# Kernel tuning notes

Hardware: AMD Instinct MI355X
Metric: run time of the kernel (lower is better)

## Reference

```python
import jax, jax.numpy as jnp
import numpy as np

B, S, D, H = 4, 1024, 1024, 16
DH = D // H
LN_EPS = 1e-5


def setup_inputs() -> dict:
    key = jax.random.key(0)
    ks = jax.random.split(key, 12)
    lim = 1.0 / np.sqrt(D)
    u = lambda k, shp: jax.random.uniform(k, shp, jnp.float32, -lim, lim)
    return {
        "x": jax.random.normal(ks[0], (B, S, D), jnp.float32),
        "Wq": u(ks[1], (D, D)), "bq": u(ks[2], (D,)),
        "Wk": u(ks[3], (D, D)), "bk": u(ks[4], (D,)),
        "Wv": u(ks[5], (D, D)), "bv": u(ks[6], (D,)),
        "Wo": u(ks[7], (D, D)), "bo": u(ks[8], (D,)),
        "gamma": jnp.ones((D,), jnp.float32),
        "beta": jnp.zeros((D,), jnp.float32),
    }


def _layer_norm(x, gamma, beta):
    mu = jnp.mean(x, axis=-1, keepdims=True)
    var = jnp.mean(jnp.square(x - mu), axis=-1, keepdims=True)
    return (x - mu) * jax.lax.rsqrt(var + LN_EPS) * gamma + beta


def reference(x, Wq, bq, Wk, bk, Wv, bv, Wo, bo, gamma, beta):
    # Linear projections (torch Linear: x @ W^T + b)
    Q = x @ Wq.T + bq  # [B, S, D]
    K = x @ Wk.T + bk
    V = x @ Wv.T + bv
    # Faithful to original: raw view(B*H, S, DH) with NO head transpose
    Q = Q.reshape(B * H, S, DH)
    K = K.reshape(B * H, S, DH)
    V = V.reshape(B * H, S, DH)
    scale = DH ** -0.5
    attn = jnp.einsum('bqd,bkd->bqk', Q, K) * scale  # [B*H, S, S]
    attn = jax.nn.softmax(attn, axis=-1)
    ctx = jnp.einsum('bqk,bkd->bqd', attn, V)  # [B*H, S, DH]
    ctx = ctx.reshape(B, S, D)
    out = ctx @ Wo.T + bo
    out = out + x  # residual (dropout p=0.0 is identity)
    return _layer_norm(out, gamma, beta)
```

## Files before the change

### kernel.cpp

```cpp
#include <hip/hip_runtime.h>
#include <hip/hip_bf16.h>


using u16 = unsigned short;
typedef __attribute__((ext_vector_type(8))) short bf16x8;
typedef __attribute__((ext_vector_type(4))) float f32x4;
typedef __attribute__((ext_vector_type(4))) u16  u16x4;
typedef __attribute__((ext_vector_type(8))) u16  u16x8;

#define AS1C(p) ((const __attribute__((address_space(1))) void*)(p))
#define AS3(p)  ((__attribute__((address_space(3))) void*)(p))

__device__ __forceinline__ u16 f2bf(float f) {
  union { float f; unsigned u; } v; v.f = f;
  unsigned u = v.u;
  return (u16)((u + 0x7fffu + ((u >> 16) & 1u)) >> 16);
}

__device__ __forceinline__ f32x4 mfma16(bf16x8 a, bf16x8 b, f32x4 c) {
  return __builtin_amdgcn_mfma_f32_16x16x32_bf16(a, b, c, 0, 0, 0);
}

__global__ __launch_bounds__(256) void prep_kernel(
    const float* __restrict__ x,
    const float* __restrict__ wq, const float* __restrict__ wk,
    const float* __restrict__ wv, const float* __restrict__ wo,
    const float* __restrict__ bq, const float* __restrict__ bk, const float* __restrict__ bv,
    u16* __restrict__ xb, u16* __restrict__ wb, float* __restrict__ bc)
{
  int ch = blockIdx.x * 256 + threadIdx.x;
  if (ch < 2097152) {
    const float* src; u16* dst;
    if (ch < 1048576) { src = x + ch * 4; dst = xb + ch * 4; }
    else {
      int c2 = ch - 1048576;
      int wsel = c2 >> 18;
      int off  = c2 & 262143;
      const float* wsrc[4] = { wq, wk, wv, wo };
      src = wsrc[wsel] + off * 4;
      dst = wb + wsel * 1048576 + off * 4;
    }
    f32x4 v = *(const f32x4*)src;
    u16x4 o;
    o[0] = f2bf(v[0]); o[1] = f2bf(v[1]); o[2] = f2bf(v[2]); o[3] = f2bf(v[3]);
    *(u16x4*)dst = o;
  } else {
    int c3 = ch - 2097152;
    int bsel = c3 >> 8, off = c3 & 255;
    const float* bsrc[3] = { bq, bk, bv };
    f32x4 v = *(const f32x4*)(bsrc[bsel] + off * 4);
    *(f32x4*)(bc + bsel * 1024 + off * 4) = v;
  }
}

template <int MODE>
__global__ __launch_bounds__(256) void gemm_p4(
    const u16* __restrict__ A, const u16* __restrict__ Bw,
    const float* __restrict__ bias, const float* __restrict__ resid,
    u16* __restrict__ outb, float* __restrict__ outf)
{
  __shared__ u16 As[3][4096];
  __shared__ u16 Bs[3][4096];

  const int K = 1024;
  int tid = threadIdx.x, w = tid >> 6, lane = tid & 63;
  int g = lane >> 4, lr = lane & 15;
  int wr = w >> 1, wcn = w & 1;

  int bid = blockIdx.x;
  int bm = (bid & 7) + 8 * ((bid >> 3) & 3);
  int bn = bid >> 5;

  int ch0 = tid, ch1 = tid + 256;
  auto srcoff = [&](int ch) -> size_t {
    int r = ch >> 2, pc = ch & 3;
    int gc = pc ^ ((r >> 2) & 3);
    return (size_t)r * K + gc * 8;
  };
  const u16* aS0 = A  + (size_t)(bm * 128) * K + srcoff(ch0);
  const u16* aS1 = A  + (size_t)(bm * 128) * K + srcoff(ch1);
  const u16* bS0 = Bw + (size_t)(bn * 128) * K + srcoff(ch0);
  const u16* bS1 = Bw + (size_t)(bn * 128) * K + srcoff(ch1);
  int lo0 = ch0 * 8, lo1 = ch1 * 8;

  auto STAGE = [&](int buf, int kt) {
    __builtin_amdgcn_global_load_lds(AS1C(aS0 + kt * 32), AS3(&As[buf][lo0]), 16, 0, 0);
    __builtin_amdgcn_global_load_lds(AS1C(aS1 + kt * 32), AS3(&As[buf][lo1]), 16, 0, 0);
    __builtin_amdgcn_global_load_lds(AS1C(bS0 + kt * 32), AS3(&Bs[buf][lo0]), 16, 0, 0);
    __builtin_amdgcn_global_load_lds(AS1C(bS1 + kt * 32), AS3(&Bs[buf][lo1]), 16, 0, 0);
  };

  f32x4 acc[4][4] = {};
  int pc8 = (g ^ ((lr >> 2) & 3)) * 8;

  auto COMPUTE = [&](int buf) {
    bf16x8 af[4], bfr[4];
#pragma unroll
    for (int m = 0; m < 4; ++m)
      af[m] = *(const bf16x8*)&As[buf][(wr * 64 + m * 16 + lr) * 32 + pc8];
#pragma unroll
    for (int n = 0; n < 4; ++n)
      bfr[n] = *(const bf16x8*)&Bs[buf][(wcn * 64 + n * 16 + lr) * 32 + pc8];
    __builtin_amdgcn_s_setprio(1);
#pragma unroll
    for (int m = 0; m < 4; ++m)
#pragma unroll
      for (int n = 0; n < 4; ++n)
        acc[m][n] = mfma16(af[m], bfr[n], acc[m][n]);
    __builtin_amdgcn_s_setprio(0);
  };

  STAGE(0, 0); STAGE(1, 1);

  int sb = 2;
  int cb = 0;
  for (int t = 0; t < 31; ++t) {
    asm volatile("s_waitcnt vmcnt(4)" ::: "memory");
    __builtin_amdgcn_s_barrier();
    asm volatile("" ::: "memory");
    if (t < 30) {
      STAGE(sb, t + 2);
      if (++sb == 3) sb = 0;
    }
    COMPUTE(cb);
    if (++cb == 3) cb = 0;
  }
  asm volatile("s_waitcnt vmcnt(0)" ::: "memory");
  __builtin_amdgcn_s_barrier();
  asm volatile("" ::: "memory");
  COMPUTE(cb);

#pragma unroll
  for (int m = 0; m < 4; ++m) {
    int row0 = bm * 128 + wr * 64 + m * 16 + 4 * g;
#pragma unroll
    for (int n = 0; n < 4; ++n) {
      int col = bn * 128 + wcn * 64 + n * 16 + lr;
#pragma unroll
      for (int i = 0; i < 4; ++i) {
        float v = acc[m][n][i];
        if (MODE == 0) {
          v += bias[col];
          int r = row0 + i;
          if (col < 1024) {
            outb[(size_t)r * 1024 + col] = f2bf(v * 0.125f);
          } else if (col < 2048) {
            outb[4194304 + (size_t)r * 1024 + (col - 1024)] = f2bf(v);
          } else {
            int c = col - 2048;
            outb[8388608 + (size_t)(r >> 6) * 65536 + (size_t)(c & 63) * 1024
                 + (r & 63) * 16 + (c >> 6)] = f2bf(v);
          }
        } else {
          size_t idx = (size_t)(row0 + i) * 1024 + col;
          outf[idx] = v + bias[col] + resid[idx];
        }
      }
    }
  }
}

__global__ __launch_bounds__(512) void attn_kernel(
    const u16* __restrict__ Qb, const u16* __restrict__ Kb,
    const u16* __restrict__ Vtb, u16* __restrict__ Ob)
{
  __shared__ u16 Ks[2][64 * 64];
  __shared__ u16 Vts[2][64 * 64];
  __shared__ u16 Ps[8][16 * 72];

  int blk = blockIdx.x;
  int bh = blk & 63, qt = blk >> 6;
  int tid = threadIdx.x, wid = tid >> 6, lane = tid & 63;
  int g = lane >> 4, lr = lane & 15;

  const u16* Qp = Qb  + (size_t)bh * 65536;
  const u16* Kp = Kb  + (size_t)bh * 65536;
  const u16* Vp = Vtb + (size_t)bh * 65536;

  bf16x8 qf[2];
#pragma unroll
  for (int f = 0; f < 2; ++f)
    qf[f] = *(const bf16x8*)&Qp[(size_t)(qt * 128 + wid * 16 + lr) * 64 + f * 32 + 8 * g];

  f32x4 oacc[4] = {};
  float mrow[4], lrowv[4];
#pragma unroll
  for (int i = 0; i < 4; ++i) { mrow[i] = -1e30f; lrowv[i] = 0.f; }

  int kc  = tid >> 3, scc = tid & 7;
  const u16* gkBase = Kp + (size_t)kc * 64 + (size_t)(scc ^ (kc & 7)) * 8;
  const u16* gvBase = Vp + (size_t)kc * 1024 + (size_t)(scc ^ (kc & 7)) * 8;

#define STAGE_ATTN(b, kt) do { \
    __builtin_amdgcn_global_load_lds(AS1C(gkBase + (size_t)(kt) * 4096), AS3(&Ks[b][tid * 8]),  16, 0, 0); \
    __builtin_amdgcn_global_load_lds(AS1C(gvBase + (kt) * 64),           AS3(&Vts[b][tid * 8]), 16, 0, 0); \
  } while (0)

  STAGE_ATTN(0, 0);
  __syncthreads();
  int cur = 0;

  for (int kt = 0; kt < 16; ++kt) {
    if (kt + 1 < 16) STAGE_ATTN(cur ^ 1, kt + 1);

    f32x4 s[4];
#pragma unroll
    for (int n = 0; n < 4; ++n) {
      f32x4 z = { 0.f, 0.f, 0.f, 0.f };
      int kr = n * 16 + lr;
#pragma unroll
      for (int f = 0; f < 2; ++f) {
        bf16x8 kb = *(const bf16x8*)&Ks[cur][kr * 64 + (((f * 4 + g) ^ (kr & 7)) * 8)];
        z = mfma16(qf[f], kb, z);
      }
      s[n] = z;
    }

    float corr[4], pvv[4][4];
#pragma unroll
    for (int i = 0; i < 4; ++i) {
      float tm = fmaxf(fmaxf(s[0][i], s[1][i]), fmaxf(s[2][i], s[3][i]));
#pragma unroll
      for (int ms = 1; ms < 16; ms <<= 1) tm = fmaxf(tm, __shfl_xor(tm, ms));
      float mn = fmaxf(mrow[i], tm);
      corr[i] = __expf(mrow[i] - mn);
      float rs = 0.f;
#pragma unroll
      for (int n = 0; n < 4; ++n) {
        float p = __expf(s[n][i] - mn);
        pvv[n][i] = p; rs += p;
      }
#pragma unroll
      for (int ms = 1; ms < 16; ms <<= 1) rs += __shfl_xor(rs, ms);
      lrowv[i] = lrowv[i] * corr[i] + rs;
      mrow[i] = mn;
    }
#pragma unroll
    for (int nd = 0; nd < 4; ++nd) {
      f32x4 o = oacc[nd];
      o[0] *= corr[0]; o[1] *= corr[1]; o[2] *= corr[2]; o[3] *= corr[3];
      oacc[nd] = o;
    }

#pragma unroll
    for (int n = 0; n < 4; ++n)
#pragma unroll
      for (int i = 0; i < 4; ++i)
        Ps[wid][(4 * g + i) * 72 + n * 16 + lr] = f2bf(pvv[n][i]);
    asm volatile("s_waitcnt lgkmcnt(0)" ::: "memory");

#pragma unroll
    for (int f = 0; f < 2; ++f) {
      bf16x8 pa = *(const bf16x8*)&Ps[wid][lr * 72 + f * 32 + 8 * g];
#pragma unroll
      for (int nd = 0; nd < 4; ++nd) {
        int dr = nd * 16 + lr;
        bf16x8 vb = *(const bf16x8*)&Vts[cur][dr * 64 + (((f * 4 + g) ^ (dr & 7)) * 8)];
        oacc[nd] = mfma16(pa, vb, oacc[nd]);
      }
    }
    __syncthreads();
    cur ^= 1;
  }

  u16* Op = Ob + (size_t)bh * 65536 + (size_t)(qt * 128 + wid * 16) * 64;
#pragma unroll
  for (int nd = 0; nd < 4; ++nd)
#pragma unroll
    for (int i = 0; i < 4; ++i)
      Op[(4 * g + i) * 64 + nd * 16 + lr] = f2bf(oacc[nd][i] / lrowv[i]);
}

__global__ __launch_bounds__(256) void ln_kernel(
    float* __restrict__ out, const float* __restrict__ gamma, const float* __restrict__ beta)
{
  int row = blockIdx.x, tid = threadIdx.x;
  int lane = tid & 63, wid = tid >> 6;
  f32x4 v = *(const f32x4*)&out[(size_t)row * 1024 + tid * 4];
  float s = v[0] + v[1] + v[2] + v[3];
  float q = v[0] * v[0] + v[1] * v[1] + v[2] * v[2] + v[3] * v[3];
#pragma unroll
  for (int ms = 1; ms < 64; ms <<= 1) { s += __shfl_xor(s, ms); q += __shfl_xor(q, ms); }
  __shared__ float red[8];
  if (lane == 0) { red[wid] = s; red[wid + 4] = q; }
  __syncthreads();
  s = red[0] + red[1] + red[2] + red[3];
  q = red[4] + red[5] + red[6] + red[7];
  float mu = s * (1.f / 1024.f);
  float var = q * (1.f / 1024.f) - mu * mu;
  float inv = rsqrtf(var + 1e-5f);
  f32x4 g4 = *(const f32x4*)&gamma[tid * 4];
  f32x4 b4 = *(const f32x4*)&beta[tid * 4];
  f32x4 o;
#pragma unroll
  for (int j = 0; j < 4; ++j) o[j] = (v[j] - mu) * inv * g4[j] + b4[j];
  *(f32x4*)&out[(size_t)row * 1024 + tid * 4] = o;
}

extern "C" void kernel_launch(void* const* d_in, const int* in_sizes, int n_in,
                              void* d_out, int out_size, void* d_ws, size_t ws_size,
                              hipStream_t stream) {
  const float* x     = (const float*)d_in[0];
  const float* Wq    = (const float*)d_in[1];
  const float* bq    = (const float*)d_in[2];
  const float* Wk    = (const float*)d_in[3];
  const float* bk    = (const float*)d_in[4];
  const float* Wv    = (const float*)d_in[5];
  const float* bv    = (const float*)d_in[6];
  const float* Wo    = (const float*)d_in[7];
  const float* bo    = (const float*)d_in[8];
  const float* gamma = (const float*)d_in[9];
  const float* beta  = (const float*)d_in[10];
  float* out = (float*)d_out;

  char* ws = (char*)d_ws;
  u16*   xb  = (u16*)ws;
  u16*   wb  = (u16*)(ws + (8u << 20));
  float* bc  = (float*)(ws + (16u << 20));
  u16*   qkv = (u16*)(ws + (16u << 20) + 16384);
  u16*   ctx = xb;

  prep_kernel<<<8195, 256, 0, stream>>>(x, Wq, Wk, Wv, Wo, bq, bk, bv, xb, wb, bc);

  gemm_p4<0><<<768, 256, 0, stream>>>(xb, wb, bc, nullptr, qkv, nullptr);

  attn_kernel<<<512, 512, 0, stream>>>(qkv, qkv + 4194304, qkv + 8388608, ctx);

  gemm_p4<1><<<256, 256, 0, stream>>>(ctx, wb + 3 * 1048576, bo, x, nullptr, out);

  ln_kernel<<<4096, 256, 0, stream>>>(out, gamma, beta);
}
```

Baseline: 145.9 us.

## Use 256x256 8-wave QKV GEMM and smaller-M tiles for output projection

Replaces the shared templated GEMM with two specialized kernels. The QKV projection now uses 256x256 tiles with 512 threads, K-step 64, double buffering and interleaved sub-tile staging and MFMA phases, which raises operand reuse per LDS load. The output projection drops to 64x128 tiles so its grid grows from 256 to 512 blocks and fills the device better. The cost is heavier register pressure, many barriers per K-step in the QKV kernel, and only 192 blocks for that GEMM, which may underfill the CUs.

Result: slower. 161.5 us (+10.7%).

```diff
diff --git a/kernel.cpp b/kernel.cpp
--- a/kernel.cpp
+++ b/kernel.cpp
@@ -20,6 +20,8 @@
 __device__ __forceinline__ f32x4 mfma16(bf16x8 a, bf16x8 b, f32x4 c) {
   return __builtin_amdgcn_mfma_f32_16x16x32_bf16(a, b, c, 0, 0, 0);
 }
+
+#define BARRIER() do { asm volatile("" ::: "memory"); __builtin_amdgcn_s_barrier(); asm volatile("" ::: "memory"); } while (0)
 
 __global__ __launch_bounds__(256) void prep_kernel(
     const float* __restrict__ x,
@@ -53,57 +55,174 @@
   }
 }
 
-template <int MODE>
-__global__ __launch_bounds__(256) void gemm_p4(
+__global__ __launch_bounds__(512, 2) void gemm_qkv(
+    const u16* __restrict__ A, const u16* __restrict__ Bw,
+    const float* __restrict__ bias, u16* __restrict__ outb)
+{
+  __shared__ u16 As[2][2][8192];
+  __shared__ u16 Bs[2][2][8192];
+
+  const int K = 1024;
+  int tid = threadIdx.x, w = tid >> 6, lane = tid & 63;
+  int g = lane >> 4, lr = lane & 15;
+  int wr = w >> 2, wc = w & 3;
+  int bid = blockIdx.x;
+  int bm = bid & 15, bn = bid >> 4;
+
+  int r0 = tid >> 3;
+  int c0 = ((tid & 7) ^ (r0 & 7)) * 8;
+  const u16* Abase = A  + (size_t)(bm * 256) * K;
+  const u16* Bbase = Bw + (size_t)(bn * 256) * K;
+
+  auto stageA = [&](int slot, int h, int kt) {
+    const u16* s0 = Abase + (size_t)(h * 128 + r0) * K + kt * 64 + c0;
+    u16* dst = &As[slot][h][tid * 8];
+    __builtin_amdgcn_global_load_lds(AS1C(s0),            AS3(dst),        16, 0, 0);
+    __builtin_amdgcn_global_load_lds(AS1C(s0 + 64 * K),   AS3(dst + 4096), 16, 0, 0);
+  };
+  auto stageB = [&](int slot, int h, int kt) {
+    const u16* s0 = Bbase + (size_t)(h * 128 + r0) * K + kt * 64 + c0;
+    u16* dst = &Bs[slot][h][tid * 8];
+    __builtin_amdgcn_global_load_lds(AS1C(s0),            AS3(dst),        16, 0, 0);
+    __builtin_amdgcn_global_load_lds(AS1C(s0 + 64 * K),   AS3(dst + 4096), 16, 0, 0);
+  };
+
+  f32x4 acc[8][4] = {};
+  bf16x8 af[4][2], bf[4][2];
+  int rsw = (lr & 7) * 8;
+
+  auto LDA = [&](int slot, int mb) {
+#pragma unroll
+    for (int mm = 0; mm < 4; ++mm)
+#pragma unroll
+      for (int kk = 0; kk < 2; ++kk)
+        af[mm][kk] = *(const bf16x8*)&As[slot][wr][(mb + mm) * 1024 + lr * 64 + ((kk * 32 + g * 8) ^ rsw)];
+  };
+  auto LDB = [&](int slot, int nb) {
+#pragma unroll
+    for (int nn = 0; nn < 2; ++nn)
+#pragma unroll
+      for (int kk = 0; kk < 2; ++kk)
+        bf[nb + nn][kk] = *(const bf16x8*)&Bs[slot][wc >> 1][((wc & 1) * 64 + (nb + nn) * 16 + lr) * 64 + ((kk * 32 + g * 8) ^ rsw)];
+  };
+  auto MF = [&](int mb, int nb) {
+    __builtin_amdgcn_s_setprio(1);
+#pragma unroll
+    for (int mm = 0; mm < 4; ++mm)
+#pragma unroll
+      for (int nn = 0; nn < 2; ++nn)
+#pragma unroll
+        for (int kk = 0; kk < 2; ++kk)
+          acc[mb + mm][nb + nn] = mfma16(af[mm][kk], bf[nb + nn][kk], acc[mb + mm][nb + nn]);
+    __builtin_amdgcn_s_setprio(0);
+  };
+
+  stageA(0, 0, 0); stageA(0, 1, 0);
+  stageB(0, 0, 0); stageB(0, 1, 0);
+  stageB(1, 0, 1); stageB(1, 1, 1);
+  asm volatile("s_waitcnt vmcnt(4)" ::: "memory");
+  BARRIER();
+
+  for (int t = 0; t < 16; ++t) {
+    int d = t & 1;
+    LDA(d, 0); LDB(d, 0);
+    if (t + 1 < 16) stageA(d ^ 1, 0, t + 1);
+    BARRIER();
+    asm volatile("s_waitcnt lgkmcnt(0)" ::: "memory");
+    __builtin_amdgcn_sched_barrier(0);
+    MF(0, 0);
+    BARRIER();
+    LDB(d, 2);
+    if (t + 1 < 16) stageA(d ^ 1, 1, t + 1);
+    BARRIER();
+    asm volatile("s_waitcnt lgkmcnt(0)" ::: "memory");
+    __builtin_amdgcn_sched_barrier(0);
+    MF(0, 2);
+    BARRIER();
+    LDA(d, 4);
+    if (t + 2 < 16) stageB(d, 0, t + 2);
+    BARRIER();
+    asm volatile("s_waitcnt lgkmcnt(0)" ::: "memory");
+    __builtin_amdgcn_sched_barrier(0);
+    MF(4, 2);
+    BARRIER();
+    if (t + 2 < 16) stageB(d, 1, t + 2);
+    if (t < 14) { asm volatile("s_waitcnt vmcnt(4)" ::: "memory"); }
+    else        { asm volatile("s_waitcnt vmcnt(0)" ::: "memory"); }
+    BARRIER();
+    __builtin_amdgcn_sched_barrier(0);
+    MF(4, 0);
+    BARRIER();
+  }
+
+#pragma unroll
+  for (int m = 0; m < 8; ++m) {
+    int row0 = bm * 256 + wr * 128 + m * 16 + 4 * g;
+#pragma unroll
+    for (int n = 0; n < 4; ++n) {
+      int col = bn * 256 + wc * 64 + n * 16 + lr;
+#pragma unroll
+      for (int i = 0; i < 4; ++i) {
+        float v = acc[m][n][i] + bias[col];
+        int r = row0 + i;
+        if (col < 1024) {
+          outb[(size_t)r * 1024 + col] = f2bf(v * 0.125f);
+        } else if (col < 2048) {
+          outb[4194304 + (size_t)r * 1024 + (col - 1024)] = f2bf(v);
+        } else {
+          int c = col - 2048;
+          outb[8388608 + (size_t)(r >> 6) * 65536 + (size_t)(c & 63) * 1024
+               + (r & 63) * 16 + (c >> 6)] = f2bf(v);
+        }
+      }
+    }
+  }
+}
+
+__global__ __launch_bounds__(256) void gemm_op(
     const u16* __restrict__ A, const u16* __restrict__ Bw,
     const float* __restrict__ bias, const float* __restrict__ resid,
-    u16* __restrict__ outb, float* __restrict__ outf)
+    float* __restrict__ outf)
 {
-  __shared__ u16 As[3][4096];
+  __shared__ u16 As[3][2048];
   __shared__ u16 Bs[3][4096];
 
   const int K = 1024;
   int tid = threadIdx.x, w = tid >> 6, lane = tid & 63;
   int g = lane >> 4, lr = lane & 15;
   int wr = w >> 1, wcn = w & 1;
-
   int bid = blockIdx.x;
-  int bm = (bid & 7) + 8 * ((bid >> 3) & 3);
-  int bn = bid >> 5;
-
-  int ch0 = tid, ch1 = tid + 256;
+  int bm = bid & 63, bn = bid >> 6;
+
   auto srcoff = [&](int ch) -> size_t {
     int r = ch >> 2, pc = ch & 3;
     int gc = pc ^ ((r >> 2) & 3);
     return (size_t)r * K + gc * 8;
   };
-  const u16* aS0 = A  + (size_t)(bm * 128) * K + srcoff(ch0);
-  const u16* aS1 = A  + (size_t)(bm * 128) * K + srcoff(ch1);
-  const u16* bS0 = Bw + (size_t)(bn * 128) * K + srcoff(ch0);
-  const u16* bS1 = Bw + (size_t)(bn * 128) * K + srcoff(ch1);
-  int lo0 = ch0 * 8, lo1 = ch1 * 8;
+  const u16* aS0 = A  + (size_t)(bm * 64)  * K + srcoff(tid);
+  const u16* bS0 = Bw + (size_t)(bn * 128) * K + srcoff(tid);
+  const u16* bS1 = Bw + (size_t)(bn * 128) * K + srcoff(tid + 256);
 
   auto STAGE = [&](int buf, int kt) {
-    __builtin_amdgcn_global_load_lds(AS1C(aS0 + kt * 32), AS3(&As[buf][lo0]), 16, 0, 0);
-    __builtin_amdgcn_global_load_lds(AS1C(aS1 + kt * 32), AS3(&As[buf][lo1]), 16, 0, 0);
-    __builtin_amdgcn_global_load_lds(AS1C(bS0 + kt * 32), AS3(&Bs[buf][lo0]), 16, 0, 0);
-    __builtin_amdgcn_global_load_lds(AS1C(bS1 + kt * 32), AS3(&Bs[buf][lo1]), 16, 0, 0);
-  };
-
-  f32x4 acc[4][4] = {};
+    __builtin_amdgcn_global_load_lds(AS1C(aS0 + kt * 32), AS3(&As[buf][tid * 8]),        16, 0, 0);
+    __builtin_amdgcn_global_load_lds(AS1C(bS0 + kt * 32), AS3(&Bs[buf][tid * 8]),        16, 0, 0);
+    __builtin_amdgcn_global_load_lds(AS1C(bS1 + kt * 32), AS3(&Bs[buf][2048 + tid * 8]), 16, 0, 0);
+  };
+
+  f32x4 acc[2][4] = {};
   int pc8 = (g ^ ((lr >> 2) & 3)) * 8;
 
   auto COMPUTE = [&](int buf) {
-    bf16x8 af[4], bfr[4];
-#pragma unroll
-    for (int m = 0; m < 4; ++m)
-      af[m] = *(const bf16x8*)&As[buf][(wr * 64 + m * 16 + lr) * 32 + pc8];
+    bf16x8 af[2], bfr[4];
+#pragma unroll
+    for (int m = 0; m < 2; ++m)
+      af[m] = *(const bf16x8*)&As[buf][(wr * 32 + m * 16 + lr) * 32 + pc8];
 #pragma unroll
     for (int n = 0; n < 4; ++n)
       bfr[n] = *(const bf16x8*)&Bs[buf][(wcn * 64 + n * 16 + lr) * 32 + pc8];
     __builtin_amdgcn_s_setprio(1);
 #pragma unroll
-    for (int m = 0; m < 4; ++m)
+    for (int m = 0; m < 2; ++m)
 #pragma unroll
       for (int n = 0; n < 4; ++n)
         acc[m][n] = mfma16(af[m], bfr[n], acc[m][n]);
@@ -112,10 +231,9 @@
 
   STAGE(0, 0); STAGE(1, 1);
 
-  int sb = 2;
-  int cb = 0;
+  int sb = 2, cb = 0;
   for (int t = 0; t < 31; ++t) {
-    asm volatile("s_waitcnt vmcnt(4)" ::: "memory");
+    asm volatile("s_waitcnt vmcnt(3)" ::: "memory");
     __builtin_amdgcn_s_barrier();
     asm volatile("" ::: "memory");
     if (t < 30) {
@@ -131,30 +249,15 @@
   COMPUTE(cb);
 
 #pragma unroll
-  for (int m = 0; m < 4; ++m) {
-    int row0 = bm * 128 + wr * 64 + m * 16 + 4 * g;
+  for (int m = 0; m < 2; ++m) {
+    int row0 = bm * 64 + wr * 32 + m * 16 + 4 * g;
 #pragma unroll
     for (int n = 0; n < 4; ++n) {
       int col = bn * 128 + wcn * 64 + n * 16 + lr;
 #pragma unroll
       for (int i = 0; i < 4; ++i) {
-        float v = acc[m][n][i];
-        if (MODE == 0) {
-          v += bias[col];
-          int r = row0 + i;
-          if (col < 1024) {
-            outb[(size_t)r * 1024 + col] = f2bf(v * 0.125f);
-          } else if (col < 2048) {
-            outb[4194304 + (size_t)r * 1024 + (col - 1024)] = f2bf(v);
-          } else {
-            int c = col - 2048;
-            outb[8388608 + (size_t)(r >> 6) * 65536 + (size_t)(c & 63) * 1024
-                 + (r & 63) * 16 + (c >> 6)] = f2bf(v);
-          }
-        } else {
-          size_t idx = (size_t)(row0 + i) * 1024 + col;
-          outf[idx] = v + bias[col] + resid[idx];
-        }
+        size_t idx = (size_t)(row0 + i) * 1024 + col;
+        outf[idx] = acc[m][n][i] + bias[col] + resid[idx];
       }
     }
   }
@@ -322,11 +425,11 @@
 
   prep_kernel<<<8195, 256, 0, stream>>>(x, Wq, Wk, Wv, Wo, bq, bk, bv, xb, wb, bc);
 
-  gemm_p4<0><<<768, 256, 0, stream>>>(xb, wb, bc, nullptr, qkv, nullptr);
+  gemm_qkv<<<192, 512, 0, stream>>>(xb, wb, bc, qkv);
 
   attn_kernel<<<512, 512, 0, stream>>>(qkv, qkv + 4194304, qkv + 8388608, ctx);
 
-  gemm_p4<1><<<256, 256, 0, stream>>>(ctx, wb + 3 * 1048576, bo, x, nullptr, out);
+  gemm_op<<<512, 256, 0, stream>>>(ctx, wb + 3 * 1048576, bo, x, out);
 
   ln_kernel<<<4096, 256, 0, stream>>>(out, gamma, beta);
 }
```

## Rewrite attention with 32x32 MFMA and register P transpose; shrink output-GEMM tiles

Applied to the files above, without the earlier changes.

The attention kernel now uses 32x32x16 MFMA with one query per lane pair, computing S^T so that row max and sum reductions are mostly in-register. P is repacked through cross-half lane shuffles instead of an LDS round trip. Blocks shrink to 128 threads with 64 queries each, giving 1024 blocks. The output projection GEMM becomes its own kernel with 64x128 tiles so 512 blocks fill more CUs. The trade-offs are higher register pressure from the f32x16 accumulators and more blocks each staging K/V tiles.

Result: faster. 134.3 us (-8.0%).

```diff
diff --git a/kernel.cpp b/kernel.cpp
--- a/kernel.cpp
+++ b/kernel.cpp
@@ -3,10 +3,12 @@
 
 
 using u16 = unsigned short;
-typedef __attribute__((ext_vector_type(8))) short bf16x8;
-typedef __attribute__((ext_vector_type(4))) float f32x4;
-typedef __attribute__((ext_vector_type(4))) u16  u16x4;
-typedef __attribute__((ext_vector_type(8))) u16  u16x8;
+using u32 = unsigned int;
+typedef __attribute__((ext_vector_type(8)))  short bf16x8;
+typedef __attribute__((ext_vector_type(4)))  float f32x4;
+typedef __attribute__((ext_vector_type(16))) float f32x16;
+typedef __attribute__((ext_vector_type(4)))  u16  u16x4;
+typedef __attribute__((ext_vector_type(8)))  u16  u16x8;
 
 #define AS1C(p) ((const __attribute__((address_space(1))) void*)(p))
 #define AS3(p)  ((__attribute__((address_space(3))) void*)(p))
@@ -19,6 +21,9 @@
 
 __device__ __forceinline__ f32x4 mfma16(bf16x8 a, bf16x8 b, f32x4 c) {
   return __builtin_amdgcn_mfma_f32_16x16x32_bf16(a, b, c, 0, 0, 0);
+}
+__device__ __forceinline__ f32x16 mfma32(bf16x8 a, bf16x8 b, f32x16 c) {
+  return __builtin_amdgcn_mfma_f32_32x32x16_bf16(a, b, c, 0, 0, 0);
 }
 
 __global__ __launch_bounds__(256) void prep_kernel(
@@ -53,11 +58,9 @@
   }
 }
 
-template <int MODE>
-__global__ __launch_bounds__(256) void gemm_p4(
+__global__ __launch_bounds__(256) void gemm_qkv(
     const u16* __restrict__ A, const u16* __restrict__ Bw,
-    const float* __restrict__ bias, const float* __restrict__ resid,
-    u16* __restrict__ outb, float* __restrict__ outf)
+    const float* __restrict__ bias, u16* __restrict__ outb)
 {
   __shared__ u16 As[3][4096];
   __shared__ u16 Bs[3][4096];
@@ -112,8 +115,7 @@
 
   STAGE(0, 0); STAGE(1, 1);
 
-  int sb = 2;
-  int cb = 0;
+  int sb = 2, cb = 0;
   for (int t = 0; t < 31; ++t) {
     asm volatile("s_waitcnt vmcnt(4)" ::: "memory");
     __builtin_amdgcn_s_barrier();
@@ -138,137 +140,248 @@
       int col = bn * 128 + wcn * 64 + n * 16 + lr;
 #pragma unroll
       for (int i = 0; i < 4; ++i) {
-        float v = acc[m][n][i];
-        if (MODE == 0) {
-          v += bias[col];
-          int r = row0 + i;
-          if (col < 1024) {
-            outb[(size_t)r * 1024 + col] = f2bf(v * 0.125f);
-          } else if (col < 2048) {
-            outb[4194304 + (size_t)r * 1024 + (col - 1024)] = f2bf(v);
-          } else {
-            int c = col - 2048;
-            outb[8388608 + (size_t)(r >> 6) * 65536 + (size_t)(c & 63) * 1024
-                 + (r & 63) * 16 + (c >> 6)] = f2bf(v);
-          }
+        float v = acc[m][n][i] + bias[col];
+        int r = row0 + i;
+        if (col < 1024) {
+          outb[(size_t)r * 1024 + col] = f2bf(v * 0.125f);
+        } else if (col < 2048) {
+          outb[4194304 + (size_t)r * 1024 + (col - 1024)] = f2bf(v);
         } else {
-          size_t idx = (size_t)(row0 + i) * 1024 + col;
-          outf[idx] = v + bias[col] + resid[idx];
+          int c = col - 2048;
+          outb[8388608 + (size_t)(r >> 6) * 65536 + (size_t)(c & 63) * 1024
+               + (r & 63) * 16 + (c >> 6)] = f2bf(v);
         }
       }
     }
   }
 }
 
-__global__ __launch_bounds__(512) void attn_kernel(
+__global__ __launch_bounds__(256) void gemm_op(
+    const u16* __restrict__ A, const u16* __restrict__ Bw,
+    const float* __restrict__ bias, const float* __restrict__ resid,
+    float* __restrict__ outf)
+{
+  __shared__ u16 As[3][2048];
+  __shared__ u16 Bs[3][4096];
+
+  const int K = 1024;
+  int tid = threadIdx.x, w = tid >> 6, lane = tid & 63;
+  int g = lane >> 4, lr = lane & 15;
+  int wr = w >> 1, wcn = w & 1;
+  int bid = blockIdx.x;
+  int bm = bid & 63, bn = bid >> 6;
+
+  auto srcoff = [&](int ch) -> size_t {
+    int r = ch >> 2, pc = ch & 3;
+    int gc = pc ^ ((r >> 2) & 3);
+    return (size_t)r * K + gc * 8;
+  };
+  const u16* aS0 = A  + (size_t)(bm * 64)  * K + srcoff(tid);
+  const u16* bS0 = Bw + (size_t)(bn * 128) * K + srcoff(tid);
+  const u16* bS1 = Bw + (size_t)(bn * 128) * K + srcoff(tid + 256);
+
+  auto STAGE = [&](int buf, int kt) {
+    __builtin_amdgcn_global_load_lds(AS1C(aS0 + kt * 32), AS3(&As[buf][tid * 8]),        16, 0, 0);
+    __builtin_amdgcn_global_load_lds(AS1C(bS0 + kt * 32), AS3(&Bs[buf][tid * 8]),        16, 0, 0);
+    __builtin_amdgcn_global_load_lds(AS1C(bS1 + kt * 32), AS3(&Bs[buf][2048 + tid * 8]), 16, 0, 0);
+  };
+
+  f32x4 acc[2][4] = {};
+  int pc8 = (g ^ ((lr >> 2) & 3)) * 8;
+
+  auto COMPUTE = [&](int buf) {
+    bf16x8 af[2], bfr[4];
+#pragma unroll
+    for (int m = 0; m < 2; ++m)
+      af[m] = *(const bf16x8*)&As[buf][(wr * 32 + m * 16 + lr) * 32 + pc8];
+#pragma unroll
+    for (int n = 0; n < 4; ++n)
+      bfr[n] = *(const bf16x8*)&Bs[buf][(wcn * 64 + n * 16 + lr) * 32 + pc8];
+    __builtin_amdgcn_s_setprio(1);
+#pragma unroll
+    for (int m = 0; m < 2; ++m)
+#pragma unroll
+      for (int n = 0; n < 4; ++n)
+        acc[m][n] = mfma16(af[m], bfr[n], acc[m][n]);
+    __builtin_amdgcn_s_setprio(0);
+  };
+
+  STAGE(0, 0); STAGE(1, 1);
+
+  int sb = 2, cb = 0;
+  for (int t = 0; t < 31; ++t) {
+    asm volatile("s_waitcnt vmcnt(3)" ::: "memory");
+    __builtin_amdgcn_s_barrier();
+    asm volatile("" ::: "memory");
+    if (t < 30) {
+      STAGE(sb, t + 2);
+      if (++sb == 3) sb = 0;
+    }
+    COMPUTE(cb);
+    if (++cb == 3) cb = 0;
+  }
+  asm volatile("s_waitcnt vmcnt(0)" ::: "memory");
+  __builtin_amdgcn_s_barrier();
+  asm volatile("" ::: "memory");
+  COMPUTE(cb);
+
+#pragma unroll
+  for (int m = 0; m < 2; ++m) {
+    int row0 = bm * 64 + wr * 32 + m * 16 + 4 * g;
+#pragma unroll
+    for (int n = 0; n < 4; ++n) {
+      int col = bn * 128 + wcn * 64 + n * 16 + lr;
+#pragma unroll
+      for (int i = 0; i < 4; ++i) {
+        size_t idx = (size_t)(row0 + i) * 1024 + col;
+        outf[idx] = acc[m][n][i] + bias[col] + resid[idx];
+      }
+    }
+  }
+}
+
+__global__ __launch_bounds__(128) void attn_kernel(
     const u16* __restrict__ Qb, const u16* __restrict__ Kb,
     const u16* __restrict__ Vtb, u16* __restrict__ Ob)
 {
-  __shared__ u16 Ks[2][64 * 64];
-  __shared__ u16 Vts[2][64 * 64];
-  __shared__ u16 Ps[8][16 * 72];
+  __shared__ u16 Ks[2][4096];
+  __shared__ u16 Vts[2][4096];
 
   int blk = blockIdx.x;
   int bh = blk & 63, qt = blk >> 6;
   int tid = threadIdx.x, wid = tid >> 6, lane = tid & 63;
-  int g = lane >> 4, lr = lane & 15;
+  int l31 = lane & 31, hi = lane >> 5;
 
   const u16* Qp = Qb  + (size_t)bh * 65536;
   const u16* Kp = Kb  + (size_t)bh * 65536;
   const u16* Vp = Vtb + (size_t)bh * 65536;
 
-  bf16x8 qf[2];
-#pragma unroll
-  for (int f = 0; f < 2; ++f)
-    qf[f] = *(const bf16x8*)&Qp[(size_t)(qt * 128 + wid * 16 + lr) * 64 + f * 32 + 8 * g];
-
-  f32x4 oacc[4] = {};
-  float mrow[4], lrowv[4];
-#pragma unroll
-  for (int i = 0; i < 4; ++i) { mrow[i] = -1e30f; lrowv[i] = 0.f; }
-
-  int kc  = tid >> 3, scc = tid & 7;
-  const u16* gkBase = Kp + (size_t)kc * 64 + (size_t)(scc ^ (kc & 7)) * 8;
-  const u16* gvBase = Vp + (size_t)kc * 1024 + (size_t)(scc ^ (kc & 7)) * 8;
-
-#define STAGE_ATTN(b, kt) do { \
-    __builtin_amdgcn_global_load_lds(AS1C(gkBase + (size_t)(kt) * 4096), AS3(&Ks[b][tid * 8]),  16, 0, 0); \
-    __builtin_amdgcn_global_load_lds(AS1C(gvBase + (kt) * 64),           AS3(&Vts[b][tid * 8]), 16, 0, 0); \
-  } while (0)
-
-  STAGE_ATTN(0, 0);
+  int q = qt * 64 + wid * 32 + l31;
+
+  bf16x8 qf[4];
+#pragma unroll
+  for (int s = 0; s < 4; ++s)
+    qf[s] = *(const bf16x8*)&Qp[(size_t)q * 64 + s * 16 + hi * 8];
+
+  f32x16 oacc[2] = {};
+  float mrow = -3e38f, lrow = 0.f;
+
+  const u16* gk[4]; const u16* gv[4];
+#pragma unroll
+  for (int j = 0; j < 4; ++j) {
+    int ch = tid + 128 * j;
+    int kc = ch >> 3, scc = ch & 7;
+    int sc = scc ^ (kc & 7);
+    gk[j] = Kp + (size_t)kc * 64   + sc * 8;
+    gv[j] = Vp + (size_t)kc * 1024 + sc * 8;
+  }
+
+#define STAGE_A(b, kt) do { \
+  _Pragma("unroll") \
+  for (int j = 0; j < 4; ++j) { \
+    int ch = tid + 128 * j; \
+    __builtin_amdgcn_global_load_lds(AS1C(gk[j] + (size_t)(kt) * 4096), AS3(&Ks[b][ch * 8]),  16, 0, 0); \
+    __builtin_amdgcn_global_load_lds(AS1C(gv[j] + (kt) * 64),           AS3(&Vts[b][ch * 8]), 16, 0, 0); \
+  } } while (0)
+
+  STAGE_A(0, 0);
   __syncthreads();
   int cur = 0;
 
   for (int kt = 0; kt < 16; ++kt) {
-    if (kt + 1 < 16) STAGE_ATTN(cur ^ 1, kt + 1);
-
-    f32x4 s[4];
-#pragma unroll
-    for (int n = 0; n < 4; ++n) {
-      f32x4 z = { 0.f, 0.f, 0.f, 0.f };
-      int kr = n * 16 + lr;
-#pragma unroll
-      for (int f = 0; f < 2; ++f) {
-        bf16x8 kb = *(const bf16x8*)&Ks[cur][kr * 64 + (((f * 4 + g) ^ (kr & 7)) * 8)];
-        z = mfma16(qf[f], kb, z);
+    if (kt + 1 < 16) STAGE_A(cur ^ 1, kt + 1);
+
+    f32x16 s2[2];
+#pragma unroll
+    for (int ks = 0; ks < 2; ++ks) {
+      f32x16 z = {};
+      int row = ks * 32 + l31;
+      int rx = (row & 7);
+#pragma unroll
+      for (int s = 0; s < 4; ++s) {
+        bf16x8 kb = *(const bf16x8*)&Ks[cur][row * 64 + (((2 * s + hi) ^ rx) * 8)];
+        z = mfma32(kb, qf[s], z);
       }
-      s[n] = z;
-    }
-
-    float corr[4], pvv[4][4];
-#pragma unroll
-    for (int i = 0; i < 4; ++i) {
-      float tm = fmaxf(fmaxf(s[0][i], s[1][i]), fmaxf(s[2][i], s[3][i]));
-#pragma unroll
-      for (int ms = 1; ms < 16; ms <<= 1) tm = fmaxf(tm, __shfl_xor(tm, ms));
-      float mn = fmaxf(mrow[i], tm);
-      corr[i] = __expf(mrow[i] - mn);
-      float rs = 0.f;
-#pragma unroll
-      for (int n = 0; n < 4; ++n) {
-        float p = __expf(s[n][i] - mn);
-        pvv[n][i] = p; rs += p;
+      s2[ks] = z;
+    }
+
+    float tv[16];
+#pragma unroll
+    for (int r = 0; r < 16; ++r) tv[r] = fmaxf(s2[0][r], s2[1][r]);
+#pragma unroll
+    for (int st = 8; st > 0; st >>= 1)
+#pragma unroll
+      for (int r = 0; r < st; ++r) tv[r] = fmaxf(tv[r], tv[r + st]);
+    float tm = fmaxf(tv[0], __shfl_xor(tv[0], 32));
+    float mn = fmaxf(mrow, tm);
+    float corr = __expf(mrow - mn);
+
+    float sv[16];
+#pragma unroll
+    for (int r = 0; r < 16; ++r) {
+      s2[0][r] = __expf(s2[0][r] - mn);
+      s2[1][r] = __expf(s2[1][r] - mn);
+      sv[r] = s2[0][r] + s2[1][r];
+    }
+#pragma unroll
+    for (int st = 8; st > 0; st >>= 1)
+#pragma unroll
+      for (int r = 0; r < st; ++r) sv[r] += sv[r + st];
+    float rs = sv[0] + __shfl_xor(sv[0], 32);
+    lrow = lrow * corr + rs;
+    mrow = mn;
+
+#pragma unroll
+    for (int dt = 0; dt < 2; ++dt)
+#pragma unroll
+      for (int r = 0; r < 16; ++r) oacc[dt][r] *= corr;
+
+    u32 wpk[2][4][2];
+#pragma unroll
+    for (int ks = 0; ks < 2; ++ks)
+#pragma unroll
+      for (int r1 = 0; r1 < 4; ++r1)
+#pragma unroll
+        for (int p = 0; p < 2; ++p)
+          wpk[ks][r1][p] = (u32)f2bf(s2[ks][4 * r1 + 2 * p])
+                         | ((u32)f2bf(s2[ks][4 * r1 + 2 * p + 1]) << 16);
+
+#pragma unroll
+    for (int s = 0; s < 4; ++s) {
+      int ks = s >> 1, t = s & 1;
+      u32 a0 = wpk[ks][2 * t][0],     a1 = wpk[ks][2 * t][1];
+      u32 b0 = wpk[ks][2 * t + 1][0], b1 = wpk[ks][2 * t + 1][1];
+      u32 sa0 = (u32)__shfl_xor((int)a0, 32), sa1 = (u32)__shfl_xor((int)a1, 32);
+      u32 sb0 = (u32)__shfl_xor((int)b0, 32), sb1 = (u32)__shfl_xor((int)b1, 32);
+      union { u32 u[4]; bf16x8 v; } pb;
+      pb.u[0] = hi ? sb0 : a0;
+      pb.u[1] = hi ? sb1 : a1;
+      pb.u[2] = hi ? b0 : sa0;
+      pb.u[3] = hi ? b1 : sa1;
+#pragma unroll
+      for (int dt = 0; dt < 2; ++dt) {
+        int row = dt * 32 + l31;
+        bf16x8 vb = *(const bf16x8*)&Vts[cur][row * 64 + (((2 * s + hi) ^ (row & 7)) * 8)];
+        oacc[dt] = mfma32(vb, pb.v, oacc[dt]);
       }
-#pragma unroll
-      for (int ms = 1; ms < 16; ms <<= 1) rs += __shfl_xor(rs, ms);
-      lrowv[i] = lrowv[i] * corr[i] + rs;
-      mrow[i] = mn;
-    }
-#pragma unroll
-    for (int nd = 0; nd < 4; ++nd) {
-      f32x4 o = oacc[nd];
-      o[0] *= corr[0]; o[1] *= corr[1]; o[2] *= corr[2]; o[3] *= corr[3];
-      oacc[nd] = o;
-    }
-
-#pragma unroll
-    for (int n = 0; n < 4; ++n)
-#pragma unroll
-      for (int i = 0; i < 4; ++i)
-        Ps[wid][(4 * g + i) * 72 + n * 16 + lr] = f2bf(pvv[n][i]);
-    asm volatile("s_waitcnt lgkmcnt(0)" ::: "memory");
-
-#pragma unroll
-    for (int f = 0; f < 2; ++f) {
-      bf16x8 pa = *(const bf16x8*)&Ps[wid][lr * 72 + f * 32 + 8 * g];
-#pragma unroll
-      for (int nd = 0; nd < 4; ++nd) {
-        int dr = nd * 16 + lr;
-        bf16x8 vb = *(const bf16x8*)&Vts[cur][dr * 64 + (((f * 4 + g) ^ (dr & 7)) * 8)];
-        oacc[nd] = mfma16(pa, vb, oacc[nd]);
-      }
-    }
+    }
+
     __syncthreads();
     cur ^= 1;
   }
 
-  u16* Op = Ob + (size_t)bh * 65536 + (size_t)(qt * 128 + wid * 16) * 64;
-#pragma unroll
-  for (int nd = 0; nd < 4; ++nd)
-#pragma unroll
-    for (int i = 0; i < 4; ++i)
-      Op[(4 * g + i) * 64 + nd * 16 + lr] = f2bf(oacc[nd][i] / lrowv[i]);
+  float inv = 1.f / lrow;
+  u16* Op = Ob + (size_t)bh * 65536 + (size_t)q * 64;
+#pragma unroll
+  for (int dt = 0; dt < 2; ++dt)
+#pragma unroll
+    for (int rq = 0; rq < 4; ++rq) {
+      int d0 = dt * 32 + 8 * rq + 4 * hi;
+      u16x4 o4;
+#pragma unroll
+      for (int rr = 0; rr < 4; ++rr) o4[rr] = f2bf(oacc[dt][4 * rq + rr] * inv);
+      *(u16x4*)&Op[d0] = o4;
+    }
 }
 
 __global__ __launch_bounds__(256) void ln_kernel(
@@ -322,11 +435,11 @@
 
   prep_kernel<<<8195, 256, 0, stream>>>(x, Wq, Wk, Wv, Wo, bq, bk, bv, xb, wb, bc);
 
-  gemm_p4<0><<<768, 256, 0, stream>>>(xb, wb, bc, nullptr, qkv, nullptr);
-
-  attn_kernel<<<512, 512, 0, stream>>>(qkv, qkv + 4194304, qkv + 8388608, ctx);
-
-  gemm_p4<1><<<256, 256, 0, stream>>>(ctx, wb + 3 * 1048576, bo, x, nullptr, out);
+  gemm_qkv<<<768, 256, 0, stream>>>(xb, wb, bc, qkv);
+
+  attn_kernel<<<1024, 128, 0, stream>>>(qkv, qkv + 4194304, qkv + 8388608, ctx);
+
+  gemm_op<<<512, 256, 0, stream>>>(ctx, wb + 3 * 1048576, bo, x, out);
 
   ln_kernel<<<4096, 256, 0, stream>>>(out, gamma, beta);
 }
```
